# Kernel optimization log

Measured on AMD Instinct MI355X. Metric: run time of the kernel, lower is better.

## Reference

```python
import jax, jax.numpy as jnp
import numpy as np
from jax.scipy.special import gammaln

EPS = 1e-8
N_SAMPLES = 2 ** 17
ATTACK_FULL_SIZE = 2048
CPD = 16
N_RES = 16
EXPR = 2
N_OSC = 2
N_GAUSS = 8
N_EVENTS = 4
FRAMES = 128
DEF_FRAMES = 128
N_LEVELS = 11  # log2(ATTACK_FULL_SIZE)


def unit_norm(x, axis=-1):
    return x / (jnp.linalg.norm(x, axis=axis, keepdims=True) + EPS)


def fft_convolve(a, b):
    # zero-pad to 2n to avoid circular wraparound, multiply spectra, crop to n
    n = a.shape[-1]
    fa = jnp.fft.rfft(a, n=2 * n, axis=-1)
    fb = jnp.fft.rfft(b, n=2 * n, axis=-1)
    return jnp.fft.irfft(fa * fb, n=2 * n, axis=-1)[..., :n]


def upsample_with_holes(x, size):
    # zero-insertion upsampling: place frames at stride `factor`
    factor = size // x.shape[-1]
    out = jnp.zeros(x.shape[:-1] + (size,), x.dtype)
    return out.at[..., ::factor].set(x)


def interpolate_last_axis(x, size):
    # linear interpolation, align_corners=False semantics (torch F.interpolate)
    n = x.shape[-1]
    scale = n / size
    src = jnp.clip((jnp.arange(size) + 0.5) * scale - 0.5, 0.0, n - 1.0)
    lo = jnp.floor(src).astype(jnp.int32)
    hi = jnp.minimum(lo + 1, n - 1)
    w = (src - lo).astype(x.dtype)
    return x[..., lo] * (1.0 - w) + x[..., hi] * w


def ensure_last_axis_length(x, size):
    n = x.shape[-1]
    if n == size:
        return x
    if n > size:
        return x[..., :size]
    return jnp.pad(x, [(0, 0)] * (x.ndim - 1) + [(0, size - n)])


def sparse_softmax(x):
    # hard one-hot forward, softmax straight-through backward
    sm = jax.nn.softmax(x, axis=-1)
    hard = jax.nn.one_hot(jnp.argmax(x, axis=-1), x.shape[-1], dtype=x.dtype)
    return hard + sm - jax.lax.stop_gradient(sm)


def hierarchical_dirac(p):
    # p: (..., L, 2) binary choices per level -> one-hot dirac of length 2**L
    sel = sparse_softmax(p)
    sig = sel[..., 0, :]
    for i in range(1, p.shape[-2]):
        sig = (sig[..., :, None] * sel[..., i, :][..., None, :]).reshape(*sig.shape[:-1], -1)
    return sig


def gamma_pdf(mean, std, n_elements):
    # gamma pdf on support (eps, 1], parameterized by mean/std
    t = jnp.linspace(EPS, 1.0, n_elements)
    k = (mean / (std + EPS)) ** 2
    rate = mean / (std ** 2 + EPS)
    k = k[..., None]
    rate = rate[..., None]
    logp = k * jnp.log(rate + EPS) + (k - 1.0) * jnp.log(t) - rate * t - gammaln(k)
    return jnp.exp(logp)


def damped_harmonic_oscillator(time, mass, damping, tension, x0):
    # underdamped closed-form solution, v0 = 0
    omega0_sq = tension / mass
    gamma = damping / (2.0 * mass)
    omega = jnp.sqrt(omega0_sq - gamma ** 2)
    A = x0
    B = gamma * x0 / omega
    return jnp.exp(-gamma * time) * (A * jnp.cos(omega * time) + B * jnp.sin(omega * time))


def dho_block(damping, mass, tension, disp, amps, tmod=None, scaling=None):
    time = jnp.linspace(0.0, 10.0, N_SAMPLES).reshape(1, 1, 1, N_SAMPLES)
    t = tension[..., None]  # (N_OSC, N_RES, EXPR, 1)
    if tmod is not None:
        t = t + tmod[0] * scaling  # broadcast -> (N_OSC, N_RES, EXPR, N_SAMPLES)
    x = damped_harmonic_oscillator(
        time,
        jax.nn.sigmoid(mass[..., None]) * 2.0,
        jax.nn.sigmoid(damping[..., None]) * 30.0,
        10.0 ** t,
        disp[..., None],
    )
    x = (x * amps).sum(axis=0)  # sum over oscillators
    return x.reshape(1, 1, N_RES, EXPR, N_SAMPLES)


def attack_envelopes(means, stds, amps, pos, overall_amp):
    m, s, a = jnp.abs(means), jnp.abs(stds), jnp.abs(amps)
    p = hierarchical_dirac(pos)  # (1,1,CPD,NG,2048)
    x = gamma_pdf(m, s, ATTACK_FULL_SIZE) * a[..., None]
    x = fft_convolve(x, p)
    x = x.sum(axis=2)  # (1,1,NG,2048)
    x = unit_norm(x)
    x = x * overall_amp[..., None]  # broadcast -> (1,1,CPD,NG,2048)
    x = x.sum(axis=-2)  # (1,1,CPD,2048)
    return x.reshape(CPD, ATTACK_FULL_SIZE)


def _forward(control_signal, deformations, ae_means, ae_stds, ae_amps, ae_pos,
             ae_overall_amp, dho_damping, dho_mass, dho_tension, dho_disp, dho_amp,
             influences, stack_mix, router, layer_mix, gains, attack_noise):
    b, ne, cpd, frames = control_signal.shape
    # --- DampedHarmonicOscillatorStack ---
    o1 = dho_block(dho_damping[0], dho_mass[0], dho_tension[0], dho_disp[0], dho_amp[0])
    o2 = dho_block(dho_damping[1], dho_mass[1], dho_tension[1], dho_disp[1], dho_amp[1], o1, influences[0])
    o3 = dho_block(dho_damping[2], dho_mass[2], dho_tension[2], dho_disp[2], dho_amp[2], o2, influences[1])
    res = (jnp.stack([o1, o2, o3], axis=-1) * jax.nn.softmax(stack_mix, axis=-1)).sum(axis=-1)
    res = unit_norm(res)
    # --- AttackEnvelopes ---
    ae = attack_envelopes(ae_means, ae_stds, ae_amps, ae_pos, ae_overall_amp)
    # --- execute_layer ---
    routed = jnp.einsum('becf,cr->berf', control_signal, router)
    before = routed
    res = unit_norm(res)  # execute_layer normalizes again
    routed = upsample_with_holes(routed.reshape(b, ne, N_RES, 1, frames), N_SAMPLES)
    # ae.shape[-1] == window_size, so materialize_attack_envelopes just multiplies noise
    impulse = ensure_last_axis_length(ae * attack_noise, N_SAMPLES).reshape(1, 1, cpd, 1, N_SAMPLES)
    routed = fft_convolve(impulse, routed)  # (1,ne,N_RES,1,S)
    cs = routed.reshape(1, ne, cpd, N_SAMPLES).sum(axis=1, keepdims=True)
    conv = fft_convolve(routed, res)  # (1,ne,N_RES,EXPR,S)
    base = jnp.zeros_like(deformations).at[:, :, 0:1, :].set(1.0)
    d = jax.nn.softmax(base + deformations, axis=-2)
    d = interpolate_last_axis(d.reshape(b, 1, 1, EXPR, -1), N_SAMPLES)
    x = (d * conv).sum(axis=-2)  # (1,ne,N_RES,S)
    mixes = jax.nn.softmax(layer_mix.reshape(1, 1, N_RES, 1, 1, 2), axis=-1)
    stacked = jnp.stack([routed, x.reshape(routed.shape)], axis=-1)
    x = (mixes * stacked).sum(axis=-1)
    x = x.reshape(1, 1, N_RES, -1)
    summed = jnp.tanh(x * jnp.abs(gains.reshape(1, 1, N_RES, 1)))
    summed = summed.sum(axis=-2, keepdims=True)
    return summed, before, cs


def setup_inputs() -> dict:
    key = jax.random.key(0)
    ks = jax.random.split(key, 20)
    u = lambda k, shape, lo, hi: jax.random.uniform(k, shape, jnp.float32, lo, hi)
    inp = {}
    inp['control_signal'] = jax.random.uniform(ks[0], (1, N_EVENTS, CPD, FRAMES), jnp.float32)
    inp['deformations'] = jax.random.normal(ks[1], (1, 1, EXPR, DEF_FRAMES), jnp.float32)
    inp['ae_means'] = u(ks[2], (1, 1, CPD, N_GAUSS), -6.0, 6.0)
    inp['ae_stds'] = u(ks[3], (1, 1, CPD, N_GAUSS), 0.5, 6.0)
    inp['ae_amps'] = u(ks[4], (1, 1, CPD, N_GAUSS), -6.0, 6.0)
    inp['ae_pos'] = u(ks[5], (1, 1, CPD, N_GAUSS, N_LEVELS, 2), -1.0, 1.0)
    inp['ae_overall_amp'] = u(ks[6], (1, 1, CPD, 1), -1.0, 1.0)
    inp['dho_damping'] = u(ks[7], (3, N_OSC, N_RES, EXPR), 0.5, 1.5)
    inp['dho_mass'] = u(ks[8], (3, N_OSC, N_RES, EXPR), -2.0, 2.0)
    inp['dho_tension'] = u(ks[9], (3, N_OSC, N_RES, EXPR), 4.0, 9.0)
    inp['dho_disp'] = u(ks[10], (3, N_OSC, N_RES, EXPR), -1.0, 2.0)
    inp['dho_amp'] = u(ks[11], (3, N_OSC, N_RES, EXPR, 1), -1.0, 1.0)
    inp['influences'] = u(ks[12], (2, N_OSC, N_RES, EXPR, 1), -0.01, 0.01)
    inp['stack_mix'] = u(ks[13], (1, 1, N_RES, EXPR, 1, 3), -1.0, 1.0)
    router = u(ks[14], (CPD, N_RES), -1.0, 1.0)
    mask = (jax.random.uniform(ks[15], (CPD, N_RES)) < 0.1).astype(jnp.float32)
    inp['router'] = router * mask
    inp['layer_mix'] = u(ks[16], (N_RES, 2), -1.0, 1.0)
    inp['gains'] = u(ks[17], (N_RES, 1), 0.01, 1.1)
    inp['attack_noise'] = u(ks[18], (CPD, ATTACK_FULL_SIZE), -1.0, 1.0)
    return inp


def reference(control_signal, deformations, ae_means, ae_stds, ae_amps, ae_pos,
              ae_overall_amp, dho_damping, dho_mass, dho_tension, dho_disp, dho_amp,
              influences, stack_mix, router, layer_mix, gains, attack_noise):
    return _forward(control_signal, deformations, ae_means, ae_stds, ae_amps, ae_pos,
                    ae_overall_amp, dho_damping, dho_mass, dho_tension, dho_disp, dho_amp,
                    influences, stack_mix, router, layer_mix, gains, attack_noise)
```

## Files before the change

### kernel.cpp

```cpp
#include <hip/hip_runtime.h>
#include <math.h>

#define NS 131072
#define EPSF 1e-8f

#define OFF_IMP    8388608u
#define OFF_VG     8421376u
#define OFF_DW     8437760u
#define OFF_FV     8568832u
#define OFF_NORM   8577024u
#define OFF_MIX0   8577064u
#define OFF_MIX1   8577080u
#define OFF_GABS   8577096u
#define OFF_PART   8578560u
#define OFF_GSSP   8594944u
#define OFF_DHP    8595200u

#define AFRAG_USH  4194304u
#define ABF2_USH   4726784u
#define HB_USH     8388608u

typedef __attribute__((ext_vector_type(8))) short short8;
typedef __attribute__((ext_vector_type(4))) float floatx4;
typedef __attribute__((ext_vector_type(4))) unsigned short ushort4v;
typedef __attribute__((ext_vector_type(4), aligned(4))) float float4u;

#define INV2PI 0.15915494309189535f

__device__ __forceinline__ float sigmf(float x) { return 1.0f / (1.0f + expf(-x)); }

__device__ __forceinline__ unsigned short f2bf(float x) {
  unsigned u = __float_as_uint(x);
  unsigned r = (u + 0x7FFFu + ((u >> 16) & 1u)) >> 16;
  return (unsigned short)r;
}

__global__ __launch_bounds__(256) void k0_params(
    const float* __restrict__ ddmp, const float* __restrict__ dmas,
    const float* __restrict__ dten, const float* __restrict__ ddisp,
    const float* __restrict__ damp, const float* __restrict__ infl,
    const float* __restrict__ smix, float* __restrict__ wsf)
{
  int tid = threadIdx.x;
  int rx = tid >> 3, ent = tid & 7;
  int r = rx >> 1, x = rx & 1;
  float* g = wsf + OFF_DHP + rx * 48;
  const double dtd = 10.0 / 131071.0;
  if (ent < 6) {
    int bb = ent >> 1, o = ent & 1;
    int id = ((bb * 2 + o) * 16 + r) * 2 + x;
    float mass = 2.0f * sigmf(dmas[id]);
    float gam = 30.0f * sigmf(ddmp[id]) / (2.0f * mass);
    double W = exp((double)dten[id] * 2.302585092994046) / (double)mass;
    float x0v = ddisp[id];
    float ampv = damp[id];
    float infv = 0.f;
    if (bb == 1) infv = infl[(o * 16 + r) * 2 + x];
    if (bb == 2) infv = infl[((2 + o) * 16 + r) * 2 + x];
    g[0 + ent]  = -gam;
    g[6 + ent]  = ampv * x0v;
    g[12 + ent] = gam * ampv * x0v;
    g[18 + ent] = infv * 2.3025851f;
    g[40 + ent] = (float)exp(-(double)gam * dtd);
    if (bb == 0) {
      double om = sqrt(W - (double)gam * (double)gam);
      g[24 + o] = (float)((double)(gam * x0v * ampv) / om);
      g[26 + o] = (float)(om * 0.15915494309189535);
      g[36 + o] = (float)sin(om * dtd);
      g[38 + o] = (float)cos(om * dtd);
    } else {
      g[28 + ent - 2] = (float)W;
    }
    if (ent == 0) { g[32] = 0.f; g[46] = 0.f; g[47] = 0.f; }
  } else if (ent == 6) {
    float a0 = smix[rx * 3], a1 = smix[rx * 3 + 1], a2 = smix[rx * 3 + 2];
    float mm = fmaxf(a0, fmaxf(a1, a2));
    float e0 = expf(a0 - mm), e1 = expf(a1 - mm), e2 = expf(a2 - mm);
    float inv = 1.0f / (e0 + e1 + e2);
    g[33] = e0 * inv; g[34] = e1 * inv; g[35] = e2 * inv;
  }
}

__global__ __launch_bounds__(256) void k01_prep_dho(
    const float* __restrict__ csig, const float* __restrict__ deform,
    const float* __restrict__ smix_unused, const float* __restrict__ router,
    const float* __restrict__ lmix, const float* __restrict__ gains,
    const float* __restrict__ means, const float* __restrict__ stds,
    const float* __restrict__ amps, const float* __restrict__ pos,
    float* __restrict__ wsf, unsigned short* __restrict__ abf2,
    unsigned short* __restrict__ resb, float* __restrict__ partials,
    float* __restrict__ out)
{
  int tid = threadIdx.x;
  int bid = blockIdx.x;
  if (bid < 512) {
    int t = bid * 256 + tid;
    {
      float src = (t + 0.5f) * (1.0f / 1024.0f) - 0.5f;
      src = fminf(fmaxf(src, 0.0f), 127.0f);
      int lo = (int)src;
      int hi = min(lo + 1, 127);
      float w = src - (float)lo;
      float c0l = 1.0f / (1.0f + expf(deform[128 + lo] - (1.0f + deform[lo])));
      float c0h = 1.0f / (1.0f + expf(deform[128 + hi] - (1.0f + deform[hi])));
      wsf[OFF_DW + t] = c0l * (1.0f - w) + c0h * w;
    }
    int mt = bid & 7, e = (bid >> 3) & 3, r = (bid >> 5) & 15;
    __shared__ float fvrow[128];
    if (tid < 128) {
      float s = 0.f;
      for (int c = 0; c < 16; ++c)
        s += csig[(e * 16 + c) * 128 + tid] * router[c * 16 + r];
      fvrow[tid] = s;
      if (mt == 0) {
        wsf[OFF_FV + (e * 16 + r) * 128 + tid] = s;
        out[524288 + (e * 16 + r) * 128 + tid] = s;
      }
    }
    __syncthreads();
    {
      int gid = bid * 256 + tid;
      int lane = gid & 63;
      int kt = (gid >> 6) & 3;
      int m = lane & 15, quad = lane >> 4;
      int base = mt * 16 + m - kt * 32 - quad * 8;
      short8 v;
#pragma unroll
      for (int j = 0; j < 8; ++j) {
        int f = base - j;
        unsigned short b = 0;
        if (f >= 0 && f < 128) b = f2bf(fvrow[f]);
        v[j] = (short)b;
      }
      *(short8*)&abf2[(size_t)gid * 8] = v;
    }
    if (bid == 0 && tid < 16) {
      int r2 = tid;
      float l0 = lmix[r2 * 2], l1 = lmix[r2 * 2 + 1];
      float mx = fmaxf(l0, l1);
      float e0 = expf(l0 - mx), e1 = expf(l1 - mx), inv = 1.0f / (e0 + e1);
      wsf[OFF_MIX0 + r2] = e0 * inv;
      wsf[OFF_MIX1 + r2] = e1 * inv;
      wsf[OFF_GABS + r2] = fabsf(gains[r2]);
    }
  } else if (bid < 576) {
    int gb = bid - 512;
    int g = gb >> 3;
    int i = (gb & 7) * 256 + tid;
    __shared__ float kS[16], rateS[16], logAS[16], aS[16];
    __shared__ int dS[16];
    __shared__ float red[4];
    if (tid < 16) {
      int c = tid, idx = c * 8 + g;
      double m = fabs((double)means[idx]);
      double s = fabs((double)stds[idx]);
      double k = m / (s + 1e-8); k = k * k;
      double rate = m / (s * s + 1e-8);
      double logA = k * log(rate + 1e-8) - lgamma(k);
      kS[c] = (float)k; rateS[c] = (float)rate; logAS[c] = (float)logA;
      aS[c] = fabsf(amps[idx]);
      int d = 0;
      for (int l = 0; l < 11; ++l) {
        float p0 = pos[(idx * 11 + l) * 2], p1 = pos[(idx * 11 + l) * 2 + 1];
        d = d * 2 + (p1 > p0 ? 1 : 0);
      }
      dS[c] = d;
    }
    __syncthreads();
    const float step = (float)((1.0 - 1e-8) / 2047.0);
    float v = 0.f;
    for (int c = 0; c < 16; ++c) {
      int mi = i - dS[c];
      if (mi >= 0) {
        float tm = 1e-8f + (float)mi * step;
        float lp = logAS[c] + (kS[c] - 1.0f) * __logf(tm) - rateS[c] * tm;
        v += aS[c] * __expf(lp);
      }
    }
    wsf[OFF_VG + g * 2048 + i] = v;
    float sumsq = v * v;
#pragma unroll
    for (int off = 32; off; off >>= 1) sumsq += __shfl_down(sumsq, off, 64);
    if ((tid & 63) == 0) red[tid >> 6] = sumsq;
    __syncthreads();
    if (tid == 0) wsf[OFF_GSSP + gb] = red[0] + red[1] + red[2] + red[3];
  } else {
    int b = bid - 576;
    int rx = b >> 6;
    int t0 = (b & 63) * 2048 + tid * 8;
    __shared__ float pf[48];
    __shared__ float bred[4];
    if (tid < 48) pf[tid] = wsf[OFF_DHP + rx * 48 + tid];
    __syncthreads();
    const float dtf = 10.0f / 131071.0f;
    float sn1[2], cn1[2], ex1[2], exd[4];
    {
      float ttf0 = (float)t0 * dtf;
#pragma unroll
      for (int o = 0; o < 2; ++o) {
        float fr = pf[26 + o] * ttf0;
        fr -= rintf(fr);
        sn1[o] = __builtin_amdgcn_sinf(fr);
        cn1[o] = __builtin_amdgcn_cosf(fr);
        ex1[o] = __expf(pf[o] * ttf0);
      }
#pragma unroll
      for (int oi = 0; oi < 4; ++oi) exd[oi] = __expf(pf[2 + oi] * ttf0);
    }
    float sqacc = 0.f;
    unsigned short h8[8];
#pragma unroll
    for (int u = 0; u < 8; ++u) {
      float ttf = (float)(t0 + u) * dtf;
      float o1v = ex1[0] * (pf[6] * cn1[0] + pf[24] * sn1[0])
                + ex1[1] * (pf[7] * cn1[1] + pf[25] * sn1[1]);
      float prev = o1v, o2v = 0.f, o3v = 0.f;
#pragma unroll
      for (int blk = 1; blk < 3; ++blk) {
        float acc = 0.f;
#pragma unroll
        for (int oo = 0; oo < 2; ++oo) {
          int o = blk * 2 + oo;
          float ng = pf[o];
          float p10 = __expf(prev * pf[18 + o]);
          float rad = __builtin_fmaf(pf[28 + o - 2], p10, -(ng * ng));
          float om = __builtin_amdgcn_sqrtf(rad);
          float fr = (om * INV2PI) * ttf;
          fr -= rintf(fr);
          float sn = __builtin_amdgcn_sinf(fr);
          float cn = __builtin_amdgcn_cosf(fr);
          float Bp = pf[12 + o] * __builtin_amdgcn_rcpf(om);
          acc += exd[o - 2] * (pf[6 + o] * cn + Bp * sn);
        }
        if (blk == 1) o2v = acc; else o3v = acc;
        prev = acc;
      }
      float rv = pf[33] * o1v + pf[34] * o2v + pf[35] * o3v;
      h8[u] = f2bf(rv);
      sqacc += rv * rv;
#pragma unroll
      for (int o = 0; o < 2; ++o) {
        float ns = sn1[o] * pf[38 + o] + cn1[o] * pf[36 + o];
        float nc = cn1[o] * pf[38 + o] - sn1[o] * pf[36 + o];
        sn1[o] = ns; cn1[o] = nc;
        ex1[o] *= pf[40 + o];
      }
#pragma unroll
      for (int oi = 0; oi < 4; ++oi) exd[oi] *= pf[42 + oi];
    }
    short8 hv;
#pragma unroll
    for (int u = 0; u < 8; ++u) hv[u] = (short)h8[u];
    *(short8*)&resb[(size_t)rx * NS + t0] = hv;
#pragma unroll
    for (int off = 32; off; off >>= 1) sqacc += __shfl_down(sqacc, off, 64);
    if ((tid & 63) == 0) bred[tid >> 6] = sqacc;
    __syncthreads();
    if (tid == 0)
      partials[rx * 512 + (b & 63)] = bred[0] + bred[1] + bred[2] + bred[3];
  }
}

__global__ __launch_bounds__(256) void kB_mid(
    const float* __restrict__ ovamp, const float* __restrict__ noise,
    float* __restrict__ wsf, unsigned short* __restrict__ abf)
{
  int bid = blockIdx.x;
  int tid = threadIdx.x;
  if (bid < 32) {
    int rx = bid;
    const float* partials = wsf + OFF_PART;
    __shared__ float red[4];
    float s = (tid < 64) ? partials[rx * 512 + tid] : 0.f;
#pragma unroll
    for (int off = 32; off; off >>= 1) s += __shfl_down(s, off, 64);
    if ((tid & 63) == 0) red[tid >> 6] = s;
    __syncthreads();
    if (tid == 0) wsf[OFF_NORM + rx] = red[0] + red[1] + red[2] + red[3];
    return;
  }
  __shared__ float wS[8];
  if (tid < 8) {
    float g8 = 0.f;
#pragma unroll
    for (int u = 0; u < 8; ++u) g8 += wsf[OFF_GSSP + tid * 8 + u];
    wS[tid] = 1.0f / (sqrtf(g8) + EPSF);
  }
  __syncthreads();
  const float* vg = wsf + OFF_VG;
  if (bid < 160) {
    int idx0 = bid - 32;
    int c = idx0 >> 3;
    int i = (idx0 & 7) * 256 + tid;
    float S = 0.f;
#pragma unroll
    for (int g = 0; g < 8; ++g) S += vg[g * 2048 + i] * wS[g];
    wsf[OFF_IMP + c * 2048 + i] = ovamp[c] * S * noise[c * 2048 + i];
    return;
  }
  int gid = (bid - 160) * 256 + tid;
  if (gid >= 66560) return;
  int r = gid / (65 * 64);
  int rem = gid % (65 * 64);
  int sc = rem >> 6, lane = rem & 63;
  int m = lane & 15, quad = lane >> 4;
  int qp = (quad < 2) ? quad : quad - 4;
  int base = 32 * sc + m - 8 * qp;
  float oa = ovamp[r];
  short8 v;
  if (base >= 7 && base < 2048) {
    float S0 = 0.f, S1 = 0.f, S2 = 0.f, S3 = 0.f, S4 = 0.f, S5 = 0.f, S6 = 0.f, S7 = 0.f;
#pragma unroll
    for (int g = 0; g < 8; ++g) {
      const float* p = vg + g * 2048 + (base - 7);
      float4u a = *(const float4u*)p;
      float4u b2 = *(const float4u*)(p + 4);
      float wg = wS[g];
      S7 = fmaf(a[0], wg, S7);  S6 = fmaf(a[1], wg, S6);
      S5 = fmaf(a[2], wg, S5);  S4 = fmaf(a[3], wg, S4);
      S3 = fmaf(b2[0], wg, S3); S2 = fmaf(b2[1], wg, S2);
      S1 = fmaf(b2[2], wg, S1); S0 = fmaf(b2[3], wg, S0);
    }
    const float* np = noise + r * 2048 + (base - 7);
    float4u na = *(const float4u*)np;
    float4u nb = *(const float4u*)(np + 4);
    v[0] = (short)f2bf(oa * S0 * nb[3]);
    v[1] = (short)f2bf(oa * S1 * nb[2]);
    v[2] = (short)f2bf(oa * S2 * nb[1]);
    v[3] = (short)f2bf(oa * S3 * nb[0]);
    v[4] = (short)f2bf(oa * S4 * na[3]);
    v[5] = (short)f2bf(oa * S5 * na[2]);
    v[6] = (short)f2bf(oa * S6 * na[1]);
    v[7] = (short)f2bf(oa * S7 * na[0]);
  } else {
#pragma unroll
    for (int j = 0; j < 8; ++j) {
      int idx = base - j;
      unsigned short b = 0;
      if (idx >= 0 && idx < 2048) {
        float S = 0.f;
#pragma unroll
        for (int g = 0; g < 8; ++g) S += vg[g * 2048 + idx] * wS[g];
        b = f2bf(oa * S * noise[r * 2048 + idx]);
      }
      v[j] = (short)b;
    }
  }
  *(short8*)&abf[(size_t)gid * 8] = v;
}

__global__ __launch_bounds__(256) void k4_mfma(
    const unsigned short* __restrict__ resb, const unsigned short* __restrict__ abf,
    const float* __restrict__ wsf, unsigned short* __restrict__ Hb)
{
  int rx = blockIdx.y, r = rx >> 1;
  int n0 = blockIdx.x * 256;
  __shared__ __align__(16) unsigned short Xs[9280];
  int tid = threadIdx.x;
  for (int i = tid; i < 772; i += 256) {
    int q_rel = i >> 1, p8 = (i & 1) * 8;
    int q = n0 - 130 + q_rel;
    short8 v = {0, 0, 0, 0, 0, 0, 0, 0};
    if (q >= 0) v = *(const short8*)&resb[(size_t)rx * NS + q * 16 + p8];
    *(short8*)&Xs[q_rel * 24 + p8] = v;
  }
  __syncthreads();
  int lane = tid & 63, w = tid >> 6;
  int quad = lane >> 4, nl = lane & 15;
  float n1 = sqrtf(wsf[OFF_NORM + rx]);
  float s1 = 1.0f / (n1 + EPSF);
  float scale = s1 * (1.0f / (n1 * s1 + EPSF)) * wsf[OFF_MIX1 + r];
  const short8* af = (const short8*)(abf) + (size_t)r * 65 * 64 + lane;
  floatx4 acc0 = {0,0,0,0}, acc1 = {0,0,0,0}, acc2 = {0,0,0,0}, acc3 = {0,0,0,0};
  const char* xbase = (const char*)Xs + (size_t)(130 + w * 64 + nl - (quad >> 1)) * 48
                      + (quad & 1) * 16;
  short8 wbuf[25];
#pragma unroll
  for (int s = -24; s < 0; ++s)
    wbuf[s + 25] = *(const short8*)(xbase - 96 * s);
#pragma unroll
  for (int sc = 0; sc < 65; ++sc) {
    wbuf[sc % 25] = *(const short8*)(xbase - 96 * sc);
    short8 a = af[sc * 64];
    acc0 = __builtin_amdgcn_mfma_f32_16x16x32_bf16(a, wbuf[sc % 25],        acc0, 0, 0, 0);
    acc1 = __builtin_amdgcn_mfma_f32_16x16x32_bf16(a, wbuf[(sc + 17) % 25], acc1, 0, 0, 0);
    acc2 = __builtin_amdgcn_mfma_f32_16x16x32_bf16(a, wbuf[(sc + 9) % 25],  acc2, 0, 0, 0);
    acc3 = __builtin_amdgcn_mfma_f32_16x16x32_bf16(a, wbuf[(sc + 1) % 25],  acc3, 0, 0, 0);
  }
  unsigned short* hp = Hb + (size_t)rx * NS + 16 * (n0 + w * 64 + nl) + quad * 4;
  ushort4v h0, h1, h2, h3;
#pragma unroll
  for (int i = 0; i < 4; ++i) {
    h0[i] = f2bf(acc0[i] * scale);
    h1[i] = f2bf(acc1[i] * scale);
    h2[i] = f2bf(acc2[i] * scale);
    h3[i] = f2bf(acc3[i] * scale);
  }
  *(ushort4v*)(hp)       = h0;
  *(ushort4v*)(hp + 256) = h1;
  *(ushort4v*)(hp + 512) = h2;
  *(ushort4v*)(hp + 768) = h3;
}

__global__ __launch_bounds__(256) void k6_mfma(
    const unsigned short* __restrict__ Hb, const float* __restrict__ imp,
    const unsigned short* __restrict__ abf2,
    const float* __restrict__ wsf, float* __restrict__ out)
{
  int rm = blockIdx.y;
  int n0 = blockIdx.x * 16;
  int zz = blockIdx.z;
  int tid = threadIdx.x;
  int wm = tid >> 6, lane = tid & 63;
  int quad = lane >> 4, n = lane & 15;
  int col = n0 + n;
  int mt = zz * 4 + wm;

  __shared__ float fvs2[4][4][128];
  for (int i = tid; i < 2048; i += 256) {
    int rq = i >> 9, e = (i >> 7) & 3, q = i & 127;
    fvs2[rq][e][q] = wsf[OFF_FV + (e * 16 + rq * 4 + rm) * 128 + q];
  }
  __syncthreads();

  float d0r[4];
  const float* dwg = wsf + OFF_DW;
#pragma unroll
  for (int i = 0; i < 4; ++i) {
    int q = mt * 16 + quad * 4 + i;
    d0r[i] = dwg[q * 1024 + col];
  }

  float tansum[4] = {0.f, 0.f, 0.f, 0.f};
  const short8* af = (const short8*)abf2;

  for (int rq = 0; rq < 4; ++rq) {
    int r = rq * 4 + rm;
    short8 bf0[4], bf1[4];
    const unsigned short* H0 = Hb + (size_t)(2 * r) * NS + col;
    const unsigned short* H1 = Hb + (size_t)(2 * r + 1) * NS + col;
#pragma unroll
    for (int kt = 0; kt < 4; ++kt) {
#pragma unroll
      for (int j = 0; j < 8; ++j) {
        int p = kt * 32 + quad * 8 + j;
        bf0[kt][j] = (short)H0[(size_t)p * 1024];
        bf1[kt][j] = (short)H1[(size_t)p * 1024];
      }
    }
    float impA = imp[r * 2048 + col];
    float impB = imp[r * 2048 + 1024 + col];
    float mix0r = wsf[OFF_MIX0 + r];
    float csum[4] = {0.f, 0.f, 0.f, 0.f};

    for (int e = 0; e < 4; ++e) {
      float ge = wsf[OFF_GABS + 4 * e + rq];
      const short8* afe = af + ((size_t)(r * 4 + e) * 32) * 64 + lane;
      floatx4 acc0 = {0, 0, 0, 0}, acc1 = {0, 0, 0, 0};
#pragma unroll
      for (int kt = 0; kt < 4; ++kt) {
        short8 a = afe[(mt * 4 + kt) * 64];
        acc0 = __builtin_amdgcn_mfma_f32_16x16x32_bf16(a, bf0[kt], acc0, 0, 0, 0);
        acc1 = __builtin_amdgcn_mfma_f32_16x16x32_bf16(a, bf1[kt], acc1, 0, 0, 0);
      }
#pragma unroll
      for (int i = 0; i < 4; ++i) {
        int q = mt * 16 + quad * 4 + i;
        float fq = fvs2[rq][e][q];
        float fqm = (q > 0) ? fvs2[rq][e][q - 1] : 0.f;
        float rsv = fq * impA + fqm * impB;
        csum[i] += rsv;
        float d0 = d0r[i];
        float conv = d0 * acc0[i] + (1.0f - d0) * acc1[i];
        float z = (mix0r * rsv + conv) * ge;
        float e2 = __expf(2.0f * z);
        tansum[i] += 1.0f - 2.0f * __builtin_amdgcn_rcpf(e2 + 1.0f);
      }
    }
#pragma unroll
    for (int i = 0; i < 4; ++i) {
      int q = mt * 16 + quad * 4 + i;
      out[532480 + (size_t)r * NS + q * 1024 + col] = csum[i];
    }
  }
#pragma unroll
  for (int i = 0; i < 4; ++i) {
    int q = mt * 16 + quad * 4 + i;
    out[(size_t)rm * NS + q * 1024 + col] = tansum[i];
  }
}

extern "C" void kernel_launch(void* const* d_in, const int* in_sizes, int n_in,
                              void* d_out, int out_size, void* d_ws, size_t ws_size,
                              hipStream_t stream) {
  const float* csig   = (const float*)d_in[0];
  const float* deform = (const float*)d_in[1];
  const float* aem    = (const float*)d_in[2];
  const float* aes    = (const float*)d_in[3];
  const float* aea    = (const float*)d_in[4];
  const float* aep    = (const float*)d_in[5];
  const float* aeo    = (const float*)d_in[6];
  const float* ddmp   = (const float*)d_in[7];
  const float* dmas   = (const float*)d_in[8];
  const float* dten   = (const float*)d_in[9];
  const float* ddisp  = (const float*)d_in[10];
  const float* damp   = (const float*)d_in[11];
  const float* infl   = (const float*)d_in[12];
  const float* smix   = (const float*)d_in[13];
  const float* router = (const float*)d_in[14];
  const float* lmix   = (const float*)d_in[15];
  const float* gains  = (const float*)d_in[16];
  const float* anoise = (const float*)d_in[17];

  float*  wsf = (float*)d_ws;
  unsigned short* resb = (unsigned short*)d_ws;
  unsigned short* abf  = (unsigned short*)d_ws + AFRAG_USH;
  unsigned short* abf2 = (unsigned short*)d_ws + ABF2_USH;
  unsigned short* Hb   = (unsigned short*)d_ws + HB_USH;
  float*  out = (float*)d_out;

  k0_params<<<1, 256, 0, stream>>>(ddmp, dmas, dten, ddisp, damp, infl, smix, wsf);
  k01_prep_dho<<<2624, 256, 0, stream>>>(csig, deform, smix, router, lmix, gains,
                                         aem, aes, aea, aep, wsf, abf2, resb,
                                         wsf + OFF_PART, out);
  kB_mid<<<420, 256, 0, stream>>>(aeo, anoise, wsf, abf);
  k4_mfma<<<dim3(32, 32), 256, 0, stream>>>(resb, abf, wsf, Hb);
  k6_mfma<<<dim3(64, 4, 2), 256, 0, stream>>>(Hb, wsf + OFF_IMP, abf2, wsf, out);
}
```

Baseline: 161.8 us.

## Regroup kernels to drop a launch, fold norm reduction into k4, stage weights in LDS

```diff
diff --git a/kernel.cpp b/kernel.cpp
--- a/kernel.cpp
+++ b/kernel.cpp
@@ -35,60 +35,16 @@
   return (unsigned short)r;
 }
 
-__global__ __launch_bounds__(256) void k0_params(
-    const float* __restrict__ ddmp, const float* __restrict__ dmas,
-    const float* __restrict__ dten, const float* __restrict__ ddisp,
-    const float* __restrict__ damp, const float* __restrict__ infl,
-    const float* __restrict__ smix, float* __restrict__ wsf)
-{
-  int tid = threadIdx.x;
-  int rx = tid >> 3, ent = tid & 7;
-  int r = rx >> 1, x = rx & 1;
-  float* g = wsf + OFF_DHP + rx * 48;
-  const double dtd = 10.0 / 131071.0;
-  if (ent < 6) {
-    int bb = ent >> 1, o = ent & 1;
-    int id = ((bb * 2 + o) * 16 + r) * 2 + x;
-    float mass = 2.0f * sigmf(dmas[id]);
-    float gam = 30.0f * sigmf(ddmp[id]) / (2.0f * mass);
-    double W = exp((double)dten[id] * 2.302585092994046) / (double)mass;
-    float x0v = ddisp[id];
-    float ampv = damp[id];
-    float infv = 0.f;
-    if (bb == 1) infv = infl[(o * 16 + r) * 2 + x];
-    if (bb == 2) infv = infl[((2 + o) * 16 + r) * 2 + x];
-    g[0 + ent]  = -gam;
-    g[6 + ent]  = ampv * x0v;
-    g[12 + ent] = gam * ampv * x0v;
-    g[18 + ent] = infv * 2.3025851f;
-    g[40 + ent] = (float)exp(-(double)gam * dtd);
-    if (bb == 0) {
-      double om = sqrt(W - (double)gam * (double)gam);
-      g[24 + o] = (float)((double)(gam * x0v * ampv) / om);
-      g[26 + o] = (float)(om * 0.15915494309189535);
-      g[36 + o] = (float)sin(om * dtd);
-      g[38 + o] = (float)cos(om * dtd);
-    } else {
-      g[28 + ent - 2] = (float)W;
-    }
-    if (ent == 0) { g[32] = 0.f; g[46] = 0.f; g[47] = 0.f; }
-  } else if (ent == 6) {
-    float a0 = smix[rx * 3], a1 = smix[rx * 3 + 1], a2 = smix[rx * 3 + 2];
-    float mm = fmaxf(a0, fmaxf(a1, a2));
-    float e0 = expf(a0 - mm), e1 = expf(a1 - mm), e2 = expf(a2 - mm);
-    float inv = 1.0f / (e0 + e1 + e2);
-    g[33] = e0 * inv; g[34] = e1 * inv; g[35] = e2 * inv;
-  }
-}
-
-__global__ __launch_bounds__(256) void k01_prep_dho(
+__global__ __launch_bounds__(256) void k01_prep(
     const float* __restrict__ csig, const float* __restrict__ deform,
-    const float* __restrict__ smix_unused, const float* __restrict__ router,
-    const float* __restrict__ lmix, const float* __restrict__ gains,
-    const float* __restrict__ means, const float* __restrict__ stds,
-    const float* __restrict__ amps, const float* __restrict__ pos,
+    const float* __restrict__ router, const float* __restrict__ lmix,
+    const float* __restrict__ gains, const float* __restrict__ means,
+    const float* __restrict__ stds, const float* __restrict__ amps,
+    const float* __restrict__ pos, const float* __restrict__ ddmp,
+    const float* __restrict__ dmas, const float* __restrict__ dten,
+    const float* __restrict__ ddisp, const float* __restrict__ damp,
+    const float* __restrict__ infl, const float* __restrict__ smix,
     float* __restrict__ wsf, unsigned short* __restrict__ abf2,
-    unsigned short* __restrict__ resb, float* __restrict__ partials,
     float* __restrict__ out)
 {
   int tid = threadIdx.x;
@@ -185,9 +141,56 @@
     __syncthreads();
     if (tid == 0) wsf[OFF_GSSP + gb] = red[0] + red[1] + red[2] + red[3];
   } else {
-    int b = bid - 576;
-    int rx = b >> 6;
-    int t0 = (b & 63) * 2048 + tid * 8;
+    int rx = tid >> 3, ent = tid & 7;
+    int r = rx >> 1, x = rx & 1;
+    float* g = wsf + OFF_DHP + rx * 48;
+    const double dtd = 10.0 / 131071.0;
+    if (ent < 6) {
+      int bb = ent >> 1, o = ent & 1;
+      int id = ((bb * 2 + o) * 16 + r) * 2 + x;
+      float mass = 2.0f * sigmf(dmas[id]);
+      float gam = 30.0f * sigmf(ddmp[id]) / (2.0f * mass);
+      double W = exp((double)dten[id] * 2.302585092994046) / (double)mass;
+      float x0v = ddisp[id];
+      float ampv = damp[id];
+      float infv = 0.f;
+      if (bb == 1) infv = infl[(o * 16 + r) * 2 + x];
+      if (bb == 2) infv = infl[((2 + o) * 16 + r) * 2 + x];
+      g[0 + ent]  = -gam;
+      g[6 + ent]  = ampv * x0v;
+      g[12 + ent] = gam * ampv * x0v;
+      g[18 + ent] = infv * 2.3025851f;
+      g[40 + ent] = (float)exp(-(double)gam * dtd);
+      if (bb == 0) {
+        double om = sqrt(W - (double)gam * (double)gam);
+        g[24 + o] = (float)((double)(gam * x0v * ampv) / om);
+        g[26 + o] = (float)(om * 0.15915494309189535);
+        g[36 + o] = (float)sin(om * dtd);
+        g[38 + o] = (float)cos(om * dtd);
+      } else {
+        g[28 + ent - 2] = (float)W;
+      }
+      if (ent == 0) { g[32] = 0.f; g[46] = 0.f; g[47] = 0.f; }
+    } else if (ent == 6) {
+      float a0 = smix[rx * 3], a1 = smix[rx * 3 + 1], a2 = smix[rx * 3 + 2];
+      float mm = fmaxf(a0, fmaxf(a1, a2));
+      float e0 = expf(a0 - mm), e1 = expf(a1 - mm), e2 = expf(a2 - mm);
+      float inv = 1.0f / (e0 + e1 + e2);
+      g[33] = e0 * inv; g[34] = e1 * inv; g[35] = e2 * inv;
+    }
+  }
+}
+
+__global__ __launch_bounds__(256) void kB_dho(
+    const float* __restrict__ ovamp, const float* __restrict__ noise,
+    float* __restrict__ wsf, unsigned short* __restrict__ abf,
+    unsigned short* __restrict__ resb, float* __restrict__ partials)
+{
+  int bid = blockIdx.x;
+  int tid = threadIdx.x;
+  if (bid < 2048) {
+    int rx = bid >> 6;
+    int t0 = (bid & 63) * 2048 + tid * 8;
     __shared__ float pf[48];
     __shared__ float bred[4];
     if (tid < 48) pf[tid] = wsf[OFF_DHP + rx * 48 + tid];
@@ -257,26 +260,7 @@
     if ((tid & 63) == 0) bred[tid >> 6] = sqacc;
     __syncthreads();
     if (tid == 0)
-      partials[rx * 512 + (b & 63)] = bred[0] + bred[1] + bred[2] + bred[3];
-  }
-}
-
-__global__ __launch_bounds__(256) void kB_mid(
-    const float* __restrict__ ovamp, const float* __restrict__ noise,
-    float* __restrict__ wsf, unsigned short* __restrict__ abf)
-{
-  int bid = blockIdx.x;
-  int tid = threadIdx.x;
-  if (bid < 32) {
-    int rx = bid;
-    const float* partials = wsf + OFF_PART;
-    __shared__ float red[4];
-    float s = (tid < 64) ? partials[rx * 512 + tid] : 0.f;
-#pragma unroll
-    for (int off = 32; off; off >>= 1) s += __shfl_down(s, off, 64);
-    if ((tid & 63) == 0) red[tid >> 6] = s;
-    __syncthreads();
-    if (tid == 0) wsf[OFF_NORM + rx] = red[0] + red[1] + red[2] + red[3];
+      partials[rx * 512 + (bid & 63)] = bred[0] + bred[1] + bred[2] + bred[3];
     return;
   }
   __shared__ float wS[8];
@@ -288,8 +272,8 @@
   }
   __syncthreads();
   const float* vg = wsf + OFF_VG;
-  if (bid < 160) {
-    int idx0 = bid - 32;
+  if (bid < 2176) {
+    int idx0 = bid - 2048;
     int c = idx0 >> 3;
     int i = (idx0 & 7) * 256 + tid;
     float S = 0.f;
@@ -298,7 +282,7 @@
     wsf[OFF_IMP + c * 2048 + i] = ovamp[c] * S * noise[c * 2048 + i];
     return;
   }
-  int gid = (bid - 160) * 256 + tid;
+  int gid = (bid - 2176) * 256 + tid;
   if (gid >= 66560) return;
   int r = gid / (65 * 64);
   int rem = gid % (65 * 64);
@@ -351,11 +335,14 @@
 
 __global__ __launch_bounds__(256) void k4_mfma(
     const unsigned short* __restrict__ resb, const unsigned short* __restrict__ abf,
-    const float* __restrict__ wsf, unsigned short* __restrict__ Hb)
+    const float* __restrict__ partials, const float* __restrict__ wsf,
+    unsigned short* __restrict__ Hb)
 {
   int rx = blockIdx.y, r = rx >> 1;
   int n0 = blockIdx.x * 256;
   __shared__ __align__(16) unsigned short Xs[9280];
+  __shared__ __align__(16) unsigned short AfS[2][832 * 8];
+  __shared__ float nrmS;
   int tid = threadIdx.x;
   for (int i = tid; i < 772; i += 256) {
     int q_rel = i >> 1, p8 = (i & 1) * 8;
@@ -364,13 +351,22 @@
     if (q >= 0) v = *(const short8*)&resb[(size_t)rx * NS + q * 16 + p8];
     *(short8*)&Xs[q_rel * 24 + p8] = v;
   }
+  const short8* afg = (const short8*)abf + (size_t)r * 65 * 64;
+  short8* afA = (short8*)AfS[0];
+  short8* afB = (short8*)AfS[1];
+  for (int i = tid; i < 832; i += 256) afA[i] = afg[i];
+  if (tid < 64) {
+    float s = partials[rx * 512 + tid];
+#pragma unroll
+    for (int off = 32; off; off >>= 1) s += __shfl_down(s, off, 64);
+    if (tid == 0) nrmS = s;
+  }
   __syncthreads();
   int lane = tid & 63, w = tid >> 6;
   int quad = lane >> 4, nl = lane & 15;
-  float n1 = sqrtf(wsf[OFF_NORM + rx]);
+  float n1 = sqrtf(nrmS);
   float s1 = 1.0f / (n1 + EPSF);
   float scale = s1 * (1.0f / (n1 * s1 + EPSF)) * wsf[OFF_MIX1 + r];
-  const short8* af = (const short8*)(abf) + (size_t)r * 65 * 64 + lane;
   floatx4 acc0 = {0,0,0,0}, acc1 = {0,0,0,0}, acc2 = {0,0,0,0}, acc3 = {0,0,0,0};
   const char* xbase = (const char*)Xs + (size_t)(130 + w * 64 + nl - (quad >> 1)) * 48
                       + (quad & 1) * 16;
@@ -379,13 +375,22 @@
   for (int s = -24; s < 0; ++s)
     wbuf[s + 25] = *(const short8*)(xbase - 96 * s);
 #pragma unroll
-  for (int sc = 0; sc < 65; ++sc) {
-    wbuf[sc % 25] = *(const short8*)(xbase - 96 * sc);
-    short8 a = af[sc * 64];
-    acc0 = __builtin_amdgcn_mfma_f32_16x16x32_bf16(a, wbuf[sc % 25],        acc0, 0, 0, 0);
-    acc1 = __builtin_amdgcn_mfma_f32_16x16x32_bf16(a, wbuf[(sc + 17) % 25], acc1, 0, 0, 0);
-    acc2 = __builtin_amdgcn_mfma_f32_16x16x32_bf16(a, wbuf[(sc + 9) % 25],  acc2, 0, 0, 0);
-    acc3 = __builtin_amdgcn_mfma_f32_16x16x32_bf16(a, wbuf[(sc + 1) % 25],  acc3, 0, 0, 0);
+  for (int c = 0; c < 5; ++c) {
+    short8* cur = (c & 1) ? afB : afA;
+    short8* nxt = (c & 1) ? afA : afB;
+    if (c < 4)
+      for (int i = tid; i < 832; i += 256) nxt[i] = afg[(c + 1) * 832 + i];
+#pragma unroll
+    for (int s5 = 0; s5 < 13; ++s5) {
+      int sc = c * 13 + s5;
+      wbuf[sc % 25] = *(const short8*)(xbase - 96 * sc);
+      short8 a = cur[s5 * 64 + lane];
+      acc0 = __builtin_amdgcn_mfma_f32_16x16x32_bf16(a, wbuf[sc % 25],        acc0, 0, 0, 0);
+      acc1 = __builtin_amdgcn_mfma_f32_16x16x32_bf16(a, wbuf[(sc + 17) % 25], acc1, 0, 0, 0);
+      acc2 = __builtin_amdgcn_mfma_f32_16x16x32_bf16(a, wbuf[(sc + 9) % 25],  acc2, 0, 0, 0);
+      acc3 = __builtin_amdgcn_mfma_f32_16x16x32_bf16(a, wbuf[(sc + 1) % 25],  acc3, 0, 0, 0);
+    }
+    __syncthreads();
   }
   unsigned short* hp = Hb + (size_t)rx * NS + 16 * (n0 + w * 64 + nl) + quad * 4;
   ushort4v h0, h1, h2, h3;
@@ -519,11 +524,10 @@
   unsigned short* Hb   = (unsigned short*)d_ws + HB_USH;
   float*  out = (float*)d_out;
 
-  k0_params<<<1, 256, 0, stream>>>(ddmp, dmas, dten, ddisp, damp, infl, smix, wsf);
-  k01_prep_dho<<<2624, 256, 0, stream>>>(csig, deform, smix, router, lmix, gains,
-                                         aem, aes, aea, aep, wsf, abf2, resb,
-                                         wsf + OFF_PART, out);
-  kB_mid<<<420, 256, 0, stream>>>(aeo, anoise, wsf, abf);
-  k4_mfma<<<dim3(32, 32), 256, 0, stream>>>(resb, abf, wsf, Hb);
+  k01_prep<<<577, 256, 0, stream>>>(csig, deform, router, lmix, gains,
+                                    aem, aes, aea, aep, ddmp, dmas, dten,
+                                    ddisp, damp, infl, smix, wsf, abf2, out);
+  kB_dho<<<2436, 256, 0, stream>>>(aeo, anoise, wsf, abf, resb, wsf + OFF_PART);
+  k4_mfma<<<dim3(32, 32), 256, 0, stream>>>(resb, abf, wsf + OFF_PART, wsf, Hb);
   k6_mfma<<<dim3(64, 4, 2), 256, 0, stream>>>(Hb, wsf + OFF_IMP, abf2, wsf, out);
 }
```

Result: no change. 161.7 us (-0.1%).
